# Kernel optimization log

Hardware: AMD Instinct MI355X
Metric: run time of the kernel (lower is better)

The kernel has to match this reference:

```python
import jax, jax.numpy as jnp
import numpy as np

B, S, H, E, K = 2, 1024, 1024, 8, 2
F = 4 * H


def setup_inputs() -> dict:
    key = jax.random.key(0)
    ks = jax.random.split(key, 8)
    std = 0.02
    return {
        "x": jax.random.normal(ks[0], (B, S, H), jnp.float32),
        "gate_w": jax.random.normal(ks[1], (E, H), jnp.float32) * (std / np.sqrt(H)),
        "gate_bias": jnp.zeros((E,), jnp.float32),
        "Wu": jax.random.normal(ks[2], (E, F, H), jnp.float32) * std,
        "bu": jnp.zeros((E, F), jnp.float32),
        "Wd": jax.random.normal(ks[3], (E, H, F), jnp.float32) * std,
        "bd": jnp.zeros((E, H), jnp.float32),
        "sWu": jax.random.normal(ks[4], (F, H), jnp.float32) * std,
        "sbu": jnp.zeros((F,), jnp.float32),
        "sWd": jax.random.normal(ks[5], (H, F), jnp.float32) * std,
        "sbd": jnp.zeros((H,), jnp.float32),
    }


def reference(x, gate_w, gate_bias, Wu, bu, Wd, bd, sWu, sbu, sWd, sbd):
    b, s, h = x.shape
    x_flat = x.reshape(-1, h)                      # [T, H]
    T = x_flat.shape[0]
    # Sigmoid gating + top-k (bias added before sigmoid, as in source)
    scores = jax.nn.sigmoid(x_flat @ gate_w.T + gate_bias)          # [T, E]
    top_scores, top_idx = jax.lax.top_k(scores, K)                  # [T, K]
    top_scores = top_scores / (top_scores.sum(-1, keepdims=True) + 1e-6)
    # Per-token per-expert combine weights (0 for non-selected experts)
    w = jnp.zeros((T, E), x.dtype).at[jnp.arange(T)[:, None], top_idx].add(top_scores)
    # Dense per-expert FFN over all tokens; masked out by w where not routed.
    h1 = jnp.einsum('th,efh->etf', x_flat, Wu) + bu[:, None, :]     # [E, T, F]
    a1 = jax.nn.gelu(h1, approximate=False)
    y = jnp.einsum('etf,ehf->eth', a1, Wd) + bd[:, None, :]         # [E, T, H]
    combined = jnp.einsum('te,eth->th', w, y)                       # [T, H]
    # Shared expert, scaled by 0.1
    sh = jax.nn.gelu(x_flat @ sWu.T + sbu, approximate=False)
    shared = (sh @ sWd.T + sbd) * 0.1
    return (combined + shared).reshape(b, s, h)
```

## Files before the change

### kernel.cpp

```cpp
#include <hip/hip_runtime.h>
#include <cstdint>
#include <cstddef>

#define T_TOK 2048
#define H_DIM 1024
#define E_NUM 8
#define F_DIM 4096
#define NG 9

typedef unsigned short ushort_t;
typedef __attribute__((ext_vector_type(8))) short bf16x8;
typedef __attribute__((ext_vector_type(4))) float f32x4;
typedef unsigned int u32;
typedef u32 __attribute__((address_space(3))) lds_u32;
typedef u32 __attribute__((address_space(1))) glob_u32;

constexpr size_t OFF_TTI = 0;
constexpr size_t OFF_TTW = 16u << 10;
constexpr size_t OFF_CNT = 32u << 10;
constexpr size_t OFF_OFFS = (32u << 10) + 256;
constexpr size_t OFF_RID = 64u << 10;
constexpr size_t OFF_WTS = 96u << 10;
constexpr size_t OFF_XBF = 1u << 20;
constexpr size_t OFF_WUB = 8u << 20;
constexpr size_t OFF_WDB = 80u << 20;
constexpr size_t OFF_A   = 152u << 20;
constexpr size_t OFF_Y   = 200u << 20;
constexpr size_t Y_SPLIT_STRIDE = (size_t)T_TOK * 3 * H_DIM;

__device__ __forceinline__ ushort_t f2bf(float f) {
  union { float f; unsigned u; } v; v.f = f;
  unsigned r = v.u + 0x7FFFu + ((v.u >> 16) & 1u);
  return (ushort_t)(r >> 16);
}

__device__ __forceinline__ float bf2f(ushort_t b) {
  union { unsigned u; float f; } v; v.u = ((unsigned)b) << 16;
  return v.f;
}

__device__ __forceinline__ float gelu_exact(float v) {
  return 0.5f * v * (1.0f + erff(v * 0.70710678118654752f));
}

__device__ __forceinline__ void gll16(const ushort_t* g, ushort_t* l) {
  __builtin_amdgcn_global_load_lds((glob_u32*)(g), (lds_u32*)(l), 16, 0, 0);
}

__global__ __launch_bounds__(256) void route_k(const float* __restrict__ x,
                                               const float* __restrict__ gw,
                                               const float* __restrict__ gb,
                                               int* __restrict__ tt_idx,
                                               float* __restrict__ tt_w) {
  const int lane = threadIdx.x & 63;
  const int wid = threadIdx.x >> 6;
  const int t = blockIdx.x * 4 + wid;
  if (t >= T_TOK) return;
  const float* xr = x + (size_t)t * H_DIM;
  float acc[8] = {0.f, 0.f, 0.f, 0.f, 0.f, 0.f, 0.f, 0.f};
  for (int i = 0; i < H_DIM; i += 64) {
    const int k = i + lane;
    const float xv = xr[k];
#pragma unroll
    for (int e = 0; e < 8; ++e) acc[e] = fmaf(xv, gw[e * H_DIM + k], acc[e]);
  }
#pragma unroll
  for (int e = 0; e < 8; ++e) {
    float v = acc[e];
#pragma unroll
    for (int s = 32; s; s >>= 1) v += __shfl_xor(v, s, 64);
    acc[e] = v;
  }
  if (lane == 0) {
    float sc[8];
#pragma unroll
    for (int e = 0; e < 8; ++e) sc[e] = 1.0f / (1.0f + expf(-(acc[e] + gb[e])));
    int i0 = 0;
#pragma unroll
    for (int e = 1; e < 8; ++e) if (sc[e] > sc[i0]) i0 = e;
    int i1 = (i0 == 0) ? 1 : 0;
#pragma unroll
    for (int e = 0; e < 8; ++e) if (e != i0 && sc[e] > sc[i1]) i1 = e;
    const float d = sc[i0] + sc[i1] + 1e-6f;
    tt_idx[2 * t] = i0;
    tt_idx[2 * t + 1] = i1;
    tt_w[2 * t] = sc[i0] / d;
    tt_w[2 * t + 1] = sc[i1] / d;
  }
}

__global__ __launch_bounds__(256) void build_k(const int* __restrict__ tt_idx,
                                               const float* __restrict__ tt_w,
                                               int* __restrict__ counts,
                                               int* __restrict__ offs,
                                               int* __restrict__ rid,
                                               float* __restrict__ wts) {
  __shared__ int cnt[NG];
  __shared__ int cur[NG];
  const int tid = threadIdx.x;
  if (tid < NG) cnt[tid] = 0;
  __syncthreads();
  for (int p = tid; p < 2 * T_TOK; p += 256) atomicAdd(&cnt[tt_idx[p]], 1);
  __syncthreads();
  if (tid == 0) {
    int run = 0;
    for (int e = 0; e < E_NUM; ++e) {
      offs[e] = run;
      counts[e] = cnt[e];
      cur[e] = run;
      run += cnt[e];
    }
    offs[E_NUM] = 2 * T_TOK;
    counts[E_NUM] = T_TOK;
    cur[E_NUM] = 2 * T_TOK;
  }
  __syncthreads();
  for (int p = tid; p < 2 * T_TOK; p += 256) {
    const int e = tt_idx[p];
    const int pos = atomicAdd(&cur[e], 1);
    rid[pos] = ((p >> 1) << 2) | (p & 1);
    wts[pos] = tt_w[p];
  }
  for (int p = tid; p < T_TOK; p += 256) {
    rid[2 * T_TOK + p] = (p << 2) | 2;
    wts[2 * T_TOK + p] = 0.1f;
  }
}

__global__ __launch_bounds__(256) void convert_k(const float* __restrict__ Wu,
                                                 const float* __restrict__ sWu,
                                                 const float* __restrict__ Wd,
                                                 const float* __restrict__ sWd,
                                                 const float* __restrict__ x,
                                                 ushort_t* __restrict__ Wub,
                                                 ushort_t* __restrict__ Wdb,
                                                 ushort_t* __restrict__ Xbf) {
  const long WE = (long)NG * F_DIM * H_DIM;
  const long W8 = (long)8 * F_DIM * H_DIM;
  const long XE = (long)T_TOK * H_DIM;
  const long total = (2 * WE + XE) / 8;
  for (long i = blockIdx.x * 256L + threadIdx.x; i < total; i += (long)gridDim.x * 256L) {
    const long base = i * 8;
    const float* src;
    ushort_t* dst;
    if (base < WE) {
      const long o = base;
      src = (o < W8) ? (Wu + o) : (sWu + (o - W8));
      dst = Wub + o;
    } else if (base < 2 * WE) {
      const long o = base - WE;
      src = (o < W8) ? (Wd + o) : (sWd + (o - W8));
      dst = Wdb + o;
    } else {
      const long o = base - 2 * WE;
      src = x + o;
      dst = Xbf + o;
    }
    const float4 v0 = *(const float4*)src;
    const float4 v1 = *(const float4*)(src + 4);
    bf16x8 r;
    r[0] = (short)f2bf(v0.x); r[1] = (short)f2bf(v0.y);
    r[2] = (short)f2bf(v0.z); r[3] = (short)f2bf(v0.w);
    r[4] = (short)f2bf(v1.x); r[5] = (short)f2bf(v1.y);
    r[6] = (short)f2bf(v1.z); r[7] = (short)f2bf(v1.w);
    *(bf16x8*)dst = r;
  }
}

__global__ __launch_bounds__(256) void up_gemm(const ushort_t* __restrict__ Xbf,
                                               const ushort_t* __restrict__ Wub,
                                               const int* __restrict__ counts,
                                               const int* __restrict__ offs,
                                               const int* __restrict__ rid,
                                               const float* __restrict__ wts,
                                               const float* __restrict__ bu,
                                               const float* __restrict__ sbu,
                                               ushort_t* __restrict__ Aout) {
  const int g = blockIdx.y >> 4;
  const int mt = blockIdx.y & 15;
  const int rows = counts[g];
  if (mt * 128 >= rows) return;
  const int off = offs[g];
  const int n0 = blockIdx.x * 128;

  __shared__ ushort_t lA[128 * 64];
  __shared__ ushort_t lB[128 * 64];

  const int tid = threadIdx.x;
  const int lane = tid & 63;
  const int wid = tid >> 6;
  const int sr = lane >> 3;
  const int swz = ((lane & 7) ^ sr) << 3;

  const ushort_t* Wg = Wub + (size_t)g * F_DIM * H_DIM;
  const ushort_t* pA[4];
  const ushort_t* pB[4];
#pragma unroll
  for (int i = 0; i < 4; ++i) {
    const int rA = (wid * 4 + i) * 8 + sr;
    int ig = mt * 128 + rA;
    if (ig >= rows) ig = rows - 1;
    pA[i] = Xbf + (size_t)(rid[off + ig] >> 2) * H_DIM + swz;
    pB[i] = Wg + (size_t)(n0 + rA) * H_DIM + swz;
  }

  f32x4 acc[4][4];
#pragma unroll
  for (int m = 0; m < 4; ++m)
#pragma unroll
    for (int n = 0; n < 4; ++n) acc[m][n] = (f32x4){0.f, 0.f, 0.f, 0.f};

  const int wr = (wid >> 1) * 64;
  const int wc = (wid & 1) * 64;
  const int fr = lane & 15;
  const int hi = lane >> 4;

  for (int k0 = 0; k0 < H_DIM; k0 += 64) {
    __syncthreads();
#pragma unroll
    for (int i = 0; i < 4; ++i) {
      gll16(pA[i] + k0, &lA[(wid * 4 + i) * 512]);
      gll16(pB[i] + k0, &lB[(wid * 4 + i) * 512]);
    }
    __syncthreads();
#pragma unroll
    for (int ks = 0; ks < 2; ++ks) {
      const int cc = ks * 4 + hi;
      bf16x8 af[4], bv[4];
#pragma unroll
      for (int m = 0; m < 4; ++m) {
        const int r = wr + m * 16 + fr;
        af[m] = *(const bf16x8*)&lA[r * 64 + ((cc ^ (r & 7)) << 3)];
      }
#pragma unroll
      for (int n = 0; n < 4; ++n) {
        const int r = wc + n * 16 + fr;
        bv[n] = *(const bf16x8*)&lB[r * 64 + ((cc ^ (r & 7)) << 3)];
      }
#pragma unroll
      for (int m = 0; m < 4; ++m)
#pragma unroll
        for (int n = 0; n < 4; ++n)
          acc[m][n] = __builtin_amdgcn_mfma_f32_16x16x32_bf16(af[m], bv[n], acc[m][n], 0, 0, 0);
    }
  }

  const float* bug = (g < E_NUM) ? (bu + (size_t)g * F_DIM) : sbu;
#pragma unroll
  for (int m = 0; m < 4; ++m) {
#pragma unroll
    for (int q = 0; q < 4; ++q) {
      const int r = wr + m * 16 + hi * 4 + q;
      const int ig = mt * 128 + r;
      if (ig < rows) {
        const float wrow = wts[off + ig];
        const size_t rowbase = (size_t)(off + ig) * F_DIM + n0;
#pragma unroll
        for (int n = 0; n < 4; ++n) {
          const int c = wc + n * 16 + fr;
          const float v = acc[m][n][q] + bug[n0 + c];
          Aout[rowbase + c] = f2bf(gelu_exact(v) * wrow);
        }
      }
    }
  }
}

__global__ __launch_bounds__(256) void down_gemm(const ushort_t* __restrict__ Ain,
                                                 const ushort_t* __restrict__ Wdb,
                                                 const int* __restrict__ counts,
                                                 const int* __restrict__ offs,
                                                 const int* __restrict__ rid,
                                                 ushort_t* __restrict__ Ybf) {
  const int g = blockIdx.y >> 4;
  const int mt = blockIdx.y & 15;
  const int rows = counts[g];
  if (mt * 128 >= rows) return;
  const int off = offs[g];
  const int n0 = blockIdx.x * 128;
  const int kbase = blockIdx.z * 2048;
  ushort_t* Ys = Ybf + (size_t)blockIdx.z * Y_SPLIT_STRIDE;

  __shared__ ushort_t lA[128 * 64];
  __shared__ ushort_t lB[128 * 64];

  const int tid = threadIdx.x;
  const int lane = tid & 63;
  const int wid = tid >> 6;
  const int sr = lane >> 3;
  const int swz = ((lane & 7) ^ sr) << 3;

  const ushort_t* Wg = Wdb + (size_t)g * H_DIM * F_DIM;
  const ushort_t* pA[4];
  const ushort_t* pB[4];
#pragma unroll
  for (int i = 0; i < 4; ++i) {
    const int rA = (wid * 4 + i) * 8 + sr;
    pA[i] = Ain + (size_t)(off + mt * 128 + rA) * F_DIM + kbase + swz;
    pB[i] = Wg + (size_t)(n0 + rA) * F_DIM + kbase + swz;
  }

  f32x4 acc[4][4];
#pragma unroll
  for (int m = 0; m < 4; ++m)
#pragma unroll
    for (int n = 0; n < 4; ++n) acc[m][n] = (f32x4){0.f, 0.f, 0.f, 0.f};

  const int wr = (wid >> 1) * 64;
  const int wc = (wid & 1) * 64;
  const int fr = lane & 15;
  const int hi = lane >> 4;

  for (int k0 = 0; k0 < 2048; k0 += 64) {
    __syncthreads();
#pragma unroll
    for (int i = 0; i < 4; ++i) {
      gll16(pA[i] + k0, &lA[(wid * 4 + i) * 512]);
      gll16(pB[i] + k0, &lB[(wid * 4 + i) * 512]);
    }
    __syncthreads();
#pragma unroll
    for (int ks = 0; ks < 2; ++ks) {
      const int cc = ks * 4 + hi;
      bf16x8 af[4], bv[4];
#pragma unroll
      for (int m = 0; m < 4; ++m) {
        const int r = wr + m * 16 + fr;
        af[m] = *(const bf16x8*)&lA[r * 64 + ((cc ^ (r & 7)) << 3)];
      }
#pragma unroll
      for (int n = 0; n < 4; ++n) {
        const int r = wc + n * 16 + fr;
        bv[n] = *(const bf16x8*)&lB[r * 64 + ((cc ^ (r & 7)) << 3)];
      }
#pragma unroll
      for (int m = 0; m < 4; ++m)
#pragma unroll
        for (int n = 0; n < 4; ++n)
          acc[m][n] = __builtin_amdgcn_mfma_f32_16x16x32_bf16(af[m], bv[n], acc[m][n], 0, 0, 0);
    }
  }

#pragma unroll
  for (int m = 0; m < 4; ++m) {
#pragma unroll
    for (int q = 0; q < 4; ++q) {
      const int r = wr + m * 16 + hi * 4 + q;
      const int ig = mt * 128 + r;
      if (ig < rows) {
        const int rv = rid[off + ig];
        ushort_t* yrow = Ys + ((size_t)(rv >> 2) * 3 + (rv & 3)) * H_DIM + n0;
#pragma unroll
        for (int n = 0; n < 4; ++n) {
          const int c = wc + n * 16 + fr;
          yrow[c] = f2bf(acc[m][n][q]);
        }
      }
    }
  }
}

__global__ __launch_bounds__(256) void combine_k(const ushort_t* __restrict__ Ybf,
                                                 const int* __restrict__ tt_idx,
                                                 const float* __restrict__ tt_w,
                                                 const float* __restrict__ bd,
                                                 const float* __restrict__ sbd,
                                                 float* __restrict__ out) {
  const int t = blockIdx.x;
  const int h = threadIdx.x * 4;
  const int e0 = tt_idx[2 * t];
  const int e1 = tt_idx[2 * t + 1];
  const float w0 = tt_w[2 * t];
  const float w1 = tt_w[2 * t + 1];
  float s[4] = {0.f, 0.f, 0.f, 0.f};
#pragma unroll
  for (int sp = 0; sp < 2; ++sp) {
#pragma unroll
    for (int sl = 0; sl < 3; ++sl) {
      const ushort_t* yp = Ybf + sp * Y_SPLIT_STRIDE + ((size_t)t * 3 + sl) * H_DIM + h;
      const ushort4 v = *(const ushort4*)yp;
      s[0] += bf2f(v.x); s[1] += bf2f(v.y); s[2] += bf2f(v.z); s[3] += bf2f(v.w);
    }
  }
  const float4 b0 = *(const float4*)(bd + (size_t)e0 * H_DIM + h);
  const float4 b1 = *(const float4*)(bd + (size_t)e1 * H_DIM + h);
  const float4 bs = *(const float4*)(sbd + h);
  float4 o;
  o.x = s[0] + w0 * b0.x + w1 * b1.x + 0.1f * bs.x;
  o.y = s[1] + w0 * b0.y + w1 * b1.y + 0.1f * bs.y;
  o.z = s[2] + w0 * b0.z + w1 * b1.z + 0.1f * bs.z;
  o.w = s[3] + w0 * b0.w + w1 * b1.w + 0.1f * bs.w;
  *(float4*)(out + (size_t)t * H_DIM + h) = o;
}

extern "C" void kernel_launch(void* const* d_in, const int* in_sizes, int n_in,
                              void* d_out, int out_size, void* d_ws, size_t ws_size,
                              hipStream_t stream) {
  (void)in_sizes; (void)n_in; (void)out_size; (void)ws_size;
  const float* x = (const float*)d_in[0];
  const float* gate_w = (const float*)d_in[1];
  const float* gate_b = (const float*)d_in[2];
  const float* Wu = (const float*)d_in[3];
  const float* bu = (const float*)d_in[4];
  const float* Wd = (const float*)d_in[5];
  const float* bd = (const float*)d_in[6];
  const float* sWu = (const float*)d_in[7];
  const float* sbu = (const float*)d_in[8];
  const float* sWd = (const float*)d_in[9];
  const float* sbd = (const float*)d_in[10];
  float* out = (float*)d_out;

  char* ws = (char*)d_ws;
  int* tt_idx = (int*)(ws + OFF_TTI);
  float* tt_w = (float*)(ws + OFF_TTW);
  int* counts = (int*)(ws + OFF_CNT);
  int* offs = (int*)(ws + OFF_OFFS);
  int* rid = (int*)(ws + OFF_RID);
  float* wts = (float*)(ws + OFF_WTS);
  ushort_t* Xbf = (ushort_t*)(ws + OFF_XBF);
  ushort_t* Wub = (ushort_t*)(ws + OFF_WUB);
  ushort_t* Wdb = (ushort_t*)(ws + OFF_WDB);
  ushort_t* A = (ushort_t*)(ws + OFF_A);
  ushort_t* Y = (ushort_t*)(ws + OFF_Y);

  hipLaunchKernelGGL(route_k, dim3(T_TOK / 4), dim3(256), 0, stream,
                     x, gate_w, gate_b, tt_idx, tt_w);
  hipLaunchKernelGGL(build_k, dim3(1), dim3(256), 0, stream,
                     tt_idx, tt_w, counts, offs, rid, wts);
  hipLaunchKernelGGL(convert_k, dim3(4096), dim3(256), 0, stream,
                     Wu, sWu, Wd, sWd, x, Wub, Wdb, Xbf);
  hipLaunchKernelGGL(up_gemm, dim3(F_DIM / 128, NG * 16), dim3(256), 0, stream,
                     Xbf, Wub, counts, offs, rid, wts, bu, sbu, A);
  hipLaunchKernelGGL(down_gemm, dim3(H_DIM / 128, NG * 16, 2), dim3(256), 0, stream,
                     A, Wdb, counts, offs, rid, Y);
  hipLaunchKernelGGL(combine_k, dim3(T_TOK), dim3(256), 0, stream,
                     Y, tt_idx, tt_w, bd, sbd, out);
}
```

Measured before the change: 593.6 us.

## Double-buffer LDS tiles in expert GEMMs and use a fast erf approximation

Both grouped GEMMs now use two LDS buffers. The next K-tile's global-to-LDS loads are issued before the MFMA work on the current tile, with a vmcnt(0) wait plus barrier between phases, so load latency overlaps compute instead of being serialised by two syncthreads per tile. The up-projection epilogue swaps erff for an Abramowitz-Stegun polynomial using a hardware reciprocal and __expf, which cuts epilogue ALU cost at some accuracy loss. LDS use per block doubles to 64KB, which may lower occupancy.

```diff
diff --git a/kernel.cpp b/kernel.cpp
--- a/kernel.cpp
+++ b/kernel.cpp
@@ -39,13 +39,29 @@
   return v.f;
 }
 
-__device__ __forceinline__ float gelu_exact(float v) {
-  return 0.5f * v * (1.0f + erff(v * 0.70710678118654752f));
+__device__ __forceinline__ float gelu_fast(float v) {
+  const float x = v * 0.70710678118654752f;
+  const float xa = fabsf(x);
+  const float t = __builtin_amdgcn_rcpf(fmaf(0.3275911f, xa, 1.0f));
+  float p = fmaf(1.061405429f, t, -1.453152027f);
+  p = fmaf(p, t, 1.421413741f);
+  p = fmaf(p, t, -0.284496736f);
+  p = fmaf(p, t, 0.254829592f);
+  p = p * t;
+  const float e = __expf(-xa * xa);
+  float erfa = fmaf(-p, e, 1.0f);
+  erfa = copysignf(erfa, x);
+  return 0.5f * v * (1.0f + erfa);
 }
 
 __device__ __forceinline__ void gll16(const ushort_t* g, ushort_t* l) {
   __builtin_amdgcn_global_load_lds((glob_u32*)(g), (lds_u32*)(l), 16, 0, 0);
 }
+
+#define VMCNT0_BARRIER do { \
+  asm volatile("s_waitcnt vmcnt(0)" ::: "memory"); \
+  __builtin_amdgcn_s_barrier(); \
+} while (0)
 
 __global__ __launch_bounds__(256) void route_k(const float* __restrict__ x,
                                                const float* __restrict__ gw,
@@ -167,6 +183,37 @@
   }
 }
 
+#define STAGE_T(A_, B_, k0_) do { \
+  _Pragma("unroll") \
+  for (int i_ = 0; i_ < 4; ++i_) { \
+    gll16(pA[i_] + (k0_), &(A_)[(wid * 4 + i_) * 512]); \
+    gll16(pB[i_] + (k0_), &(B_)[(wid * 4 + i_) * 512]); \
+  } \
+} while (0)
+
+#define COMPUTE_T(A_, B_) do { \
+  _Pragma("unroll") \
+  for (int ks_ = 0; ks_ < 2; ++ks_) { \
+    const int cc_ = ks_ * 4 + hi; \
+    bf16x8 af_[4], bv_[4]; \
+    _Pragma("unroll") \
+    for (int m_ = 0; m_ < 4; ++m_) { \
+      const int r_ = wr + m_ * 16 + fr; \
+      af_[m_] = *(const bf16x8*)&(A_)[r_ * 64 + ((cc_ ^ (r_ & 7)) << 3)]; \
+    } \
+    _Pragma("unroll") \
+    for (int n_ = 0; n_ < 4; ++n_) { \
+      const int r_ = wc + n_ * 16 + fr; \
+      bv_[n_] = *(const bf16x8*)&(B_)[r_ * 64 + ((cc_ ^ (r_ & 7)) << 3)]; \
+    } \
+    _Pragma("unroll") \
+    for (int m_ = 0; m_ < 4; ++m_) \
+      _Pragma("unroll") \
+      for (int n_ = 0; n_ < 4; ++n_) \
+        acc[m_][n_] = __builtin_amdgcn_mfma_f32_16x16x32_bf16(af_[m_], bv_[n_], acc[m_][n_], 0, 0, 0); \
+  } \
+} while (0)
+
 __global__ __launch_bounds__(256) void up_gemm(const ushort_t* __restrict__ Xbf,
                                                const ushort_t* __restrict__ Wub,
                                                const int* __restrict__ counts,
@@ -183,8 +230,7 @@
   const int off = offs[g];
   const int n0 = blockIdx.x * 128;
 
-  __shared__ ushort_t lA[128 * 64];
-  __shared__ ushort_t lB[128 * 64];
+  __shared__ ushort_t lds[4][128 * 64];
 
   const int tid = threadIdx.x;
   const int lane = tid & 63;
@@ -215,34 +261,16 @@
   const int fr = lane & 15;
   const int hi = lane >> 4;
 
-  for (int k0 = 0; k0 < H_DIM; k0 += 64) {
-    __syncthreads();
-#pragma unroll
-    for (int i = 0; i < 4; ++i) {
-      gll16(pA[i] + k0, &lA[(wid * 4 + i) * 512]);
-      gll16(pB[i] + k0, &lB[(wid * 4 + i) * 512]);
-    }
-    __syncthreads();
-#pragma unroll
-    for (int ks = 0; ks < 2; ++ks) {
-      const int cc = ks * 4 + hi;
-      bf16x8 af[4], bv[4];
-#pragma unroll
-      for (int m = 0; m < 4; ++m) {
-        const int r = wr + m * 16 + fr;
-        af[m] = *(const bf16x8*)&lA[r * 64 + ((cc ^ (r & 7)) << 3)];
-      }
-#pragma unroll
-      for (int n = 0; n < 4; ++n) {
-        const int r = wc + n * 16 + fr;
-        bv[n] = *(const bf16x8*)&lB[r * 64 + ((cc ^ (r & 7)) << 3)];
-      }
-#pragma unroll
-      for (int m = 0; m < 4; ++m)
-#pragma unroll
-        for (int n = 0; n < 4; ++n)
-          acc[m][n] = __builtin_amdgcn_mfma_f32_16x16x32_bf16(af[m], bv[n], acc[m][n], 0, 0, 0);
-    }
+  STAGE_T(lds[0], lds[1], 0);
+  VMCNT0_BARRIER;
+#pragma unroll 1
+  for (int kt = 0; kt < 16; kt += 2) {
+    STAGE_T(lds[2], lds[3], (kt + 1) * 64);
+    COMPUTE_T(lds[0], lds[1]);
+    VMCNT0_BARRIER;
+    if (kt + 2 < 16) STAGE_T(lds[0], lds[1], (kt + 2) * 64);
+    COMPUTE_T(lds[2], lds[3]);
+    VMCNT0_BARRIER;
   }
 
   const float* bug = (g < E_NUM) ? (bu + (size_t)g * F_DIM) : sbu;
@@ -259,7 +287,7 @@
         for (int n = 0; n < 4; ++n) {
           const int c = wc + n * 16 + fr;
           const float v = acc[m][n][q] + bug[n0 + c];
-          Aout[rowbase + c] = f2bf(gelu_exact(v) * wrow);
+          Aout[rowbase + c] = f2bf(gelu_fast(v) * wrow);
         }
       }
     }
@@ -281,8 +309,7 @@
   const int kbase = blockIdx.z * 2048;
   ushort_t* Ys = Ybf + (size_t)blockIdx.z * Y_SPLIT_STRIDE;
 
-  __shared__ ushort_t lA[128 * 64];
-  __shared__ ushort_t lB[128 * 64];
+  __shared__ ushort_t lds[4][128 * 64];
 
   const int tid = threadIdx.x;
   const int lane = tid & 63;
@@ -311,34 +338,16 @@
   const int fr = lane & 15;
   const int hi = lane >> 4;
 
-  for (int k0 = 0; k0 < 2048; k0 += 64) {
-    __syncthreads();
-#pragma unroll
-    for (int i = 0; i < 4; ++i) {
-      gll16(pA[i] + k0, &lA[(wid * 4 + i) * 512]);
-      gll16(pB[i] + k0, &lB[(wid * 4 + i) * 512]);
-    }
-    __syncthreads();
-#pragma unroll
-    for (int ks = 0; ks < 2; ++ks) {
-      const int cc = ks * 4 + hi;
-      bf16x8 af[4], bv[4];
-#pragma unroll
-      for (int m = 0; m < 4; ++m) {
-        const int r = wr + m * 16 + fr;
-        af[m] = *(const bf16x8*)&lA[r * 64 + ((cc ^ (r & 7)) << 3)];
-      }
-#pragma unroll
-      for (int n = 0; n < 4; ++n) {
-        const int r = wc + n * 16 + fr;
-        bv[n] = *(const bf16x8*)&lB[r * 64 + ((cc ^ (r & 7)) << 3)];
-      }
-#pragma unroll
-      for (int m = 0; m < 4; ++m)
-#pragma unroll
-        for (int n = 0; n < 4; ++n)
-          acc[m][n] = __builtin_amdgcn_mfma_f32_16x16x32_bf16(af[m], bv[n], acc[m][n], 0, 0, 0);
-    }
+  STAGE_T(lds[0], lds[1], 0);
+  VMCNT0_BARRIER;
+#pragma unroll 1
+  for (int kt = 0; kt < 32; kt += 2) {
+    STAGE_T(lds[2], lds[3], (kt + 1) * 64);
+    COMPUTE_T(lds[0], lds[1]);
+    VMCNT0_BARRIER;
+    if (kt + 2 < 32) STAGE_T(lds[0], lds[1], (kt + 2) * 64);
+    COMPUTE_T(lds[2], lds[3]);
+    VMCNT0_BARRIER;
   }
 
 #pragma unroll
```

Result: faster. 548.1 us (-7.7%).
